# Kernel optimization log

Hardware: AMD Instinct MI355X
Metric: run time of the kernel (lower is better)

The kernel has to match this reference:

```python
import jax, jax.numpy as jnp
import numpy as np

TAU = 1.0
NUM_CLASSES = 14
EDGE_W = 500.0
BODY_W = 200.0
LOSS_W = 1.0


def _cross_reduce(x, op, pad_val):
    """Apply op over the 3D 6-neighborhood cross (scipy default structure).
    x: bool [B, C, D, H, W]."""
    p = jnp.pad(x, ((0, 0), (0, 0), (1, 1), (1, 1), (1, 1)), constant_values=pad_val)
    r = p[:, :, 1:-1, 1:-1, 1:-1]
    r = op(r, p[:, :, :-2, 1:-1, 1:-1]); r = op(r, p[:, :, 2:, 1:-1, 1:-1])
    r = op(r, p[:, :, 1:-1, :-2, 1:-1]); r = op(r, p[:, :, 1:-1, 2:, 1:-1])
    r = op(r, p[:, :, 1:-1, 1:-1, :-2]); r = op(r, p[:, :, 1:-1, 1:-1, 2:])
    return r


def _edge_body_masks(gt_labels):
    # gt_labels: int [B, 1, D, H, W] -> bool masks [B, NUM_CLASSES, D, H, W]
    gt = gt_labels[:, 0]  # [B, D, H, W]
    onehot = gt[:, None] == jnp.arange(NUM_CLASSES, dtype=gt.dtype)[None, :, None, None, None]
    # binary_dilation ^ binary_erosion, both with border_value=0 (scipy default)
    dil = _cross_reduce(onehot, jnp.logical_or, False)
    ero = _cross_reduce(onehot, jnp.logical_and, False)
    edges = jnp.logical_xor(dil, ero)
    bodies = jnp.logical_and(jnp.logical_not(edges), onehot)
    # class 0 (background) masks are forced to zero in the original loop
    edges = edges.at[:, 0].set(False)
    bodies = bodies.at[:, 0].set(False)
    return edges, bodies


def _cwd(preds_S, preds_T):
    # ChannelWiseDivergence: per-(batch,channel) softmax over flattened spatial dims
    B, C = preds_S.shape[0], preds_S.shape[1]
    s = preds_S.reshape(B * C, -1) / TAU
    t = preds_T.reshape(B * C, -1) / TAU
    p_t = jax.nn.softmax(t, axis=-1)
    loss = jnp.sum(p_t * (jax.nn.log_softmax(t, axis=-1) - jax.nn.log_softmax(s, axis=-1)))
    return loss * (TAU ** 2) / (B * C)


def setup_inputs() -> dict:
    key = jax.random.key(0)
    k1, k2, k3 = jax.random.split(key, 3)
    B, C, D, H, W = 2, NUM_CLASSES, 96, 96, 96
    preds_S = jax.random.normal(k1, (B, C, D, H, W), dtype=jnp.float32)
    preds_T = jax.random.normal(k2, (B, C, D, H, W), dtype=jnp.float32)
    gt_labels = jax.random.randint(k3, (B, 1, D, H, W), 0, NUM_CLASSES, dtype=jnp.int64)
    return {"preds_S": preds_S, "preds_T": preds_T, "gt_labels": gt_labels}


def reference(preds_S, preds_T, gt_labels):
    B = preds_S.shape[0]
    edges, bodies = _edge_body_masks(gt_labels)
    me = edges.astype(preds_S.dtype)
    mb = bodies.astype(preds_S.dtype)
    loss_edges = _cwd(preds_S * me, preds_T * me) * LOSS_W * EDGE_W / B
    loss_bodies = _cwd(preds_S * mb, preds_T * mb) * LOSS_W * BODY_W / B
    return loss_edges, loss_bodies
```

## Files before the change

kernel.cpp:

```cpp
#include <hip/hip_runtime.h>
#include <math.h>

#define NCLS 14
#define DIMX 96
#define DIMXY (DIMX * DIMX)
#define NVOX (DIMX * DIMX * DIMX)
#define NVOX8 (NVOX / 8)
#define BATCH 2
#define ROWS (BATCH * NCLS)
#define TPB 256
#define CPB (TPB * 16)
#define NBLK (NVOX / CPB)

__global__ __launch_bounds__(256) void mask_kernel(const int* __restrict__ gt,
                                                   unsigned char* __restrict__ planes,
                                                   float* __restrict__ body_acc,
                                                   const float* __restrict__ Sp,
                                                   const float* __restrict__ Tp) {
    int t8 = blockIdx.x * 256 + threadIdx.x;
    if (t8 >= BATCH * NVOX8) return;
    int b = t8 / NVOX8;
    int lb = t8 - b * NVOX8;
    int v = lb * 8;
    int w = v % DIMX;
    int h = (v / DIMX) % DIMX;
    int d = v / DIMXY;
    const int* __restrict__ g = gt + (size_t)b * NVOX;

    int gc[8], up[8], dn[8], fr[8], bk[8];
    { int4 a = *(const int4*)&g[v];     int4 c2 = *(const int4*)&g[v + 4];
      gc[0]=a.x; gc[1]=a.y; gc[2]=a.z; gc[3]=a.w; gc[4]=c2.x; gc[5]=c2.y; gc[6]=c2.z; gc[7]=c2.w; }
    bool hasU = h > 0, hasD = h < DIMX - 1, hasF = d > 0, hasB = d < DIMX - 1;
    bool hasL0 = w > 0;
    bool hasR7 = w < DIMX - 8;
    if (hasU) { int4 a = *(const int4*)&g[v - DIMX];     int4 c2 = *(const int4*)&g[v - DIMX + 4];
      up[0]=a.x; up[1]=a.y; up[2]=a.z; up[3]=a.w; up[4]=c2.x; up[5]=c2.y; up[6]=c2.z; up[7]=c2.w; }
    if (hasD) { int4 a = *(const int4*)&g[v + DIMX];     int4 c2 = *(const int4*)&g[v + DIMX + 4];
      dn[0]=a.x; dn[1]=a.y; dn[2]=a.z; dn[3]=a.w; dn[4]=c2.x; dn[5]=c2.y; dn[6]=c2.z; dn[7]=c2.w; }
    if (hasF) { int4 a = *(const int4*)&g[v - DIMXY];    int4 c2 = *(const int4*)&g[v - DIMXY + 4];
      fr[0]=a.x; fr[1]=a.y; fr[2]=a.z; fr[3]=a.w; fr[4]=c2.x; fr[5]=c2.y; fr[6]=c2.z; fr[7]=c2.w; }
    if (hasB) { int4 a = *(const int4*)&g[v + DIMXY];    int4 c2 = *(const int4*)&g[v + DIMXY + 4];
      bk[0]=a.x; bk[1]=a.y; bk[2]=a.z; bk[3]=a.w; bk[4]=c2.x; bk[5]=c2.y; bk[6]=c2.z; bk[7]=c2.w; }
    int lf0 = hasL0 ? g[v - 1] : 0;
    int rt7 = hasR7 ? g[v + 8] : 0;

    unsigned e[8];
    #pragma unroll
    for (int j = 0; j < 8; ++j) {
        int c0 = gc[j];
        unsigned dil = 1u << c0;
        bool all = hasU && hasD && hasF && hasB;
        int  lf = (j == 0) ? lf0 : gc[j - 1]; bool hl = (j > 0) || hasL0;
        int  rt = (j == 7) ? rt7 : gc[j + 1]; bool hr = (j < 7) || hasR7;
        all = all && hl && hr;
        if (hl)   { dil |= 1u << lf;    all = all && (lf == c0); }
        if (hr)   { dil |= 1u << rt;    all = all && (rt == c0); }
        if (hasU) { dil |= 1u << up[j]; all = all && (up[j] == c0); }
        if (hasD) { dil |= 1u << dn[j]; all = all && (dn[j] == c0); }
        if (hasF) { dil |= 1u << fr[j]; all = all && (fr[j] == c0); }
        if (hasB) { dil |= 1u << bk[j]; all = all && (bk[j] == c0); }
        unsigned edge = dil & ~1u;
        if (all) edge &= ~(1u << c0);
        e[j] = edge;
        if (all && c0 != 0) {
            size_t off = ((size_t)(b * NCLS + c0)) * NVOX + (size_t)(v + j);
            float t = Tp[off], s = Sp[off];
            float et = __expf(t);
            float* acc = body_acc + (size_t)(b * NCLS + c0) * 4;
            atomicAdd(acc + 0, et);
            atomicAdd(acc + 1, et * (t - s));
            atomicAdd(acc + 2, __expf(s));
            atomicAdd(acc + 3, 1.f);
        }
    }
    #pragma unroll
    for (int c = 0; c < NCLS; ++c) {
        unsigned byte = 0;
        #pragma unroll
        for (int j = 0; j < 8; ++j) byte |= ((e[j] >> c) & 1u) << j;
        planes[(size_t)(b * NCLS + c) * NVOX8 + lb] = (unsigned char)byte;
    }
}

__global__ __launch_bounds__(TPB) void cwd_kernel(const float* __restrict__ Sp,
                                                  const float* __restrict__ Tp,
                                                  const unsigned char* __restrict__ planes,
                                                  float* __restrict__ partials) {
    int blk = blockIdx.x;
    int row = blk / NBLK;
    int chunk = blk - row * NBLK;
    const float* __restrict__ tp = Tp + (size_t)row * NVOX;
    const float* __restrict__ sp = Sp + (size_t)row * NVOX;
    const unsigned char* __restrict__ pl = planes + (size_t)row * NVOX8;
    int tid = (int)threadIdx.x;
    int v0 = chunk * CPB + tid * 16;

    unsigned mword = *(const unsigned short*)(pl + chunk * (CPB / 8) + tid * 2);
    const float4* __restrict__ tq = (const float4*)(tp + v0);
    const float4* __restrict__ sq = (const float4*)(sp + v0);
    float4 td0 = tq[0], td1 = tq[1], td2 = tq[2], td3 = tq[3];
    float4 sd0 = sq[0], sd1 = sq[1], sd2 = sq[2], sd3 = sq[3];

    float azt[4] = {0.f, 0.f, 0.f, 0.f};
    float as1[4] = {0.f, 0.f, 0.f, 0.f};
    float azs[4] = {0.f, 0.f, 0.f, 0.f};

    float4 tdv[4] = {td0, td1, td2, td3};
    float4 sdv[4] = {sd0, sd1, sd2, sd3};
    #pragma unroll
    for (int gi = 0; gi < 4; ++gi) {
        int g = 3 - gi;
        float tt[4] = {tdv[g].x, tdv[g].y, tdv[g].z, tdv[g].w};
        float ss[4] = {sdv[g].x, sdv[g].y, sdv[g].z, sdv[g].w};
        #pragma unroll
        for (int j = 0; j < 4; ++j) {
            bool on = (mword >> (g * 4 + j)) & 1u;
            float tv = on ? tt[j] : 0.f;
            float sv = on ? ss[j] : 0.f;
            float et = __expf(tv);
            azt[j] += et;
            as1[j] += et * (tv - sv);
            azs[j] += __expf(sv);
        }
    }

    float r0 = (azt[0] + azt[1]) + (azt[2] + azt[3]);
    float r1 = (as1[0] + as1[1]) + (as1[2] + as1[3]);
    float r2 = (azs[0] + azs[1]) + (azs[2] + azs[3]);
    #pragma unroll
    for (int off = 32; off > 0; off >>= 1) {
        r0 += __shfl_down(r0, off);
        r1 += __shfl_down(r1, off);
        r2 += __shfl_down(r2, off);
    }
    __shared__ float red[4][3];
    int wid = tid >> 6;
    int lane = tid & 63;
    if (lane == 0) { red[wid][0] = r0; red[wid][1] = r1; red[wid][2] = r2; }
    __syncthreads();
    if (tid < 3) {
        partials[(size_t)blk * 4 + tid] =
            (red[0][tid] + red[1][tid]) + (red[2][tid] + red[3][tid]);
    }
}

__global__ __launch_bounds__(1024) void final_kernel(const float* __restrict__ partials,
                                                     const float* __restrict__ body_acc,
                                                     float* __restrict__ out) {
    int tid = (int)threadIdx.x;
    int row = tid >> 5;
    int sub = tid & 31;
    __shared__ double les[ROWS], lbs[ROWS];
    if (row < ROWS) {
        double zt = 0.0, s1 = 0.0, zs = 0.0;
        for (int k = sub; k < NBLK; k += 32) {
            const float* p = partials + (size_t)(row * NBLK + k) * 4;
            zt += (double)p[0]; s1 += (double)p[1]; zs += (double)p[2];
        }
        #pragma unroll
        for (int off = 16; off > 0; off >>= 1) {
            zt += __shfl_down(zt, off, 32);
            s1 += __shfl_down(s1, off, 32);
            zs += __shfl_down(zs, off, 32);
        }
        if (sub == 0) {
            double le = s1 / zt - log(zt) + log(zs);
            const float* a = body_acc + (size_t)row * 4;
            double rem = (double)NVOX - (double)a[3];
            double bzt = (double)a[0] + rem;
            double bzs = (double)a[2] + rem;
            double lb = (double)a[1] / bzt - log(bzt) + log(bzs);
            les[row] = le;
            lbs[row] = lb;
        }
    }
    __syncthreads();
    if (tid == 0) {
        double A = 0.0, C = 0.0;
        for (int i = 0; i < ROWS; ++i) { A += les[i]; C += lbs[i]; }
        out[0] = (float)(A * (500.0 / 56.0));
        out[1] = (float)(C * (200.0 / 56.0));
    }
}

extern "C" void kernel_launch(void* const* d_in, const int* in_sizes, int n_in,
                              void* d_out, int out_size, void* d_ws, size_t ws_size,
                              hipStream_t stream) {
    const float* Sp = (const float*)d_in[0];
    const float* Tp = (const float*)d_in[1];
    const int* gt = (const int*)d_in[2];
    float* out = (float*)d_out;

    unsigned char* planes = (unsigned char*)d_ws;
    float* partials = (float*)((char*)d_ws + (size_t)ROWS * NVOX8);
    float* body_acc = partials + (size_t)ROWS * NBLK * 4;

    hipMemsetAsync(body_acc, 0, ROWS * 4 * sizeof(float), stream);
    hipLaunchKernelGGL(mask_kernel, dim3((BATCH * NVOX8 + 255) / 256), dim3(256), 0, stream,
                       gt, planes, body_acc, Sp, Tp);
    hipLaunchKernelGGL(cwd_kernel, dim3(ROWS * NBLK), dim3(TPB), 0, stream,
                       Sp, Tp, planes, partials);
    hipLaunchKernelGGL(final_kernel, dim3(1), dim3(1024), 0, stream,
                       partials, body_acc, out);
}
```

Measured before the change: 54.56 us.

## Process larger chunks per block with double-buffered inline-asm vector loads

The CWD reduction kernel now handles 16384 voxels per block instead of 4096, iterating 8 times with software double-buffered global_load_dwordx4 issued via inline asm and explicit s_waitcnt. The chunk's mask bytes are staged into LDS once per block. This aims to keep more loads in flight per thread, overlap memory latency with exp computation, and cut the number of blocks and partials. It depends on hand-written waitcnt being correct relative to other memory ops, and it reduces the total block count, which could lower occupancy.

Measured after the change: 54.25 us. About the same (-0.6%).

```diff
diff --git a/kernel.cpp b/kernel.cpp
--- a/kernel.cpp
+++ b/kernel.cpp
@@ -9,8 +9,26 @@
 #define BATCH 2
 #define ROWS (BATCH * NCLS)
 #define TPB 256
-#define CPB (TPB * 16)
-#define NBLK (NVOX / CPB)
+#define SCHUNK 16384
+#define NBLK (NVOX / SCHUNK)
+#define ITER 8
+
+typedef __attribute__((ext_vector_type(4))) float f32x4;
+
+__device__ __forceinline__ f32x4 gload(unsigned voff, const float* base) {
+    f32x4 r;
+    asm volatile("global_load_dwordx4 %0, %1, %2"
+                 : "=v"(r)
+                 : "v"(voff), "s"(base));
+    return r;
+}
+
+template <int N>
+__device__ __forceinline__ void waitload(f32x4& a, f32x4& b, f32x4& c, f32x4& d) {
+    asm volatile("s_waitcnt vmcnt(%4)"
+                 : "+v"(a), "+v"(b), "+v"(c), "+v"(d)
+                 : "n"(N));
+}
 
 __global__ __launch_bounds__(256) void mask_kernel(const int* __restrict__ gt,
                                                    unsigned char* __restrict__ planes,
@@ -91,36 +109,58 @@
     int chunk = blk - row * NBLK;
     const float* __restrict__ tp = Tp + (size_t)row * NVOX;
     const float* __restrict__ sp = Sp + (size_t)row * NVOX;
-    const unsigned char* __restrict__ pl = planes + (size_t)row * NVOX8;
+    const unsigned char* __restrict__ pl =
+        planes + (size_t)row * NVOX8 + (size_t)chunk * (SCHUNK / 8);
     int tid = (int)threadIdx.x;
-    int v0 = chunk * CPB + tid * 16;
-
-    unsigned mword = *(const unsigned short*)(pl + chunk * (CPB / 8) + tid * 2);
-    const float4* __restrict__ tq = (const float4*)(tp + v0);
-    const float4* __restrict__ sq = (const float4*)(sp + v0);
-    float4 td0 = tq[0], td1 = tq[1], td2 = tq[2], td3 = tq[3];
-    float4 sd0 = sq[0], sd1 = sq[1], sd2 = sq[2], sd3 = sq[3];
+
+    __shared__ unsigned long long mlds8[TPB];
+    mlds8[tid] = *(const unsigned long long*)(pl + tid * 8);
+    __syncthreads();
+    const unsigned char* mb = (const unsigned char*)mlds8;
+
+    unsigned base_b = (unsigned)((chunk * SCHUNK + tid * 4) * 4);
+    int mbase = tid >> 1;
+    int mshift = (tid & 1) * 4;
 
     float azt[4] = {0.f, 0.f, 0.f, 0.f};
     float as1[4] = {0.f, 0.f, 0.f, 0.f};
     float azs[4] = {0.f, 0.f, 0.f, 0.f};
 
-    float4 tdv[4] = {td0, td1, td2, td3};
-    float4 sdv[4] = {sd0, sd1, sd2, sd3};
-    #pragma unroll
-    for (int gi = 0; gi < 4; ++gi) {
-        int g = 3 - gi;
-        float tt[4] = {tdv[g].x, tdv[g].y, tdv[g].z, tdv[g].w};
-        float ss[4] = {sdv[g].x, sdv[g].y, sdv[g].z, sdv[g].w};
+    f32x4 tA[2][2], sA[2][2];
+    tA[0][0] = gload(base_b, tp);
+    tA[0][1] = gload(base_b + 4096u, tp);
+    sA[0][0] = gload(base_b, sp);
+    sA[0][1] = gload(base_b + 4096u, sp);
+
+    #pragma unroll
+    for (int i = 0; i < ITER; ++i) {
+        const int cur = i & 1, nxt = cur ^ 1;
+        if (i + 1 < ITER) {
+            unsigned vo = base_b + (unsigned)((i + 1) * 8192);
+            tA[nxt][0] = gload(vo, tp);
+            tA[nxt][1] = gload(vo + 4096u, tp);
+            sA[nxt][0] = gload(vo, sp);
+            sA[nxt][1] = gload(vo + 4096u, sp);
+            waitload<4>(tA[cur][0], tA[cur][1], sA[cur][0], sA[cur][1]);
+        } else {
+            waitload<0>(tA[cur][0], tA[cur][1], sA[cur][0], sA[cur][1]);
+        }
+        unsigned nib0 = ((unsigned)mb[i * 256 + mbase] >> mshift) & 0xFu;
+        unsigned nib1 = ((unsigned)mb[i * 256 + 128 + mbase] >> mshift) & 0xFu;
         #pragma unroll
-        for (int j = 0; j < 4; ++j) {
-            bool on = (mword >> (g * 4 + j)) & 1u;
-            float tv = on ? tt[j] : 0.f;
-            float sv = on ? ss[j] : 0.f;
-            float et = __expf(tv);
-            azt[j] += et;
-            as1[j] += et * (tv - sv);
-            azs[j] += __expf(sv);
+        for (int p = 0; p < 2; ++p) {
+            unsigned nib = p ? nib1 : nib0;
+            f32x4 t4 = tA[cur][p], s4 = sA[cur][p];
+            #pragma unroll
+            for (int j = 0; j < 4; ++j) {
+                bool on = (nib >> j) & 1u;
+                float tv = on ? t4[j] : 0.f;
+                float sv = on ? s4[j] : 0.f;
+                float et = __expf(tv);
+                azt[j] += et;
+                as1[j] += et * (tv - sv);
+                azs[j] += __expf(sv);
+            }
         }
     }
 
```
